# Performance work log

Hardware: AMD Instinct MI355X
Metric: run time of the kernel (lower is better)

## Reference

```python
import jax, jax.numpy as jnp
import numpy as np

E, N, D = 800000, 50000, 64

def setup_inputs() -> dict:
    key = jax.random.key(0)
    k0, k1, k2, k3 = jax.random.split(key, 4)
    return {
        "edge_attrs": jax.random.normal(k0, (E, D), dtype=jnp.float32),
        "proj_W": jax.random.normal(k1, (D, D), dtype=jnp.float32) / np.float32(np.sqrt(D)),
        "proj_b": jnp.zeros((D,), dtype=jnp.float32),
        "upd_W": jax.random.normal(k2, (D, D), dtype=jnp.float32) / np.float32(np.sqrt(D)),
        "upd_b": jnp.zeros((D,), dtype=jnp.float32),
        "dst": jax.random.randint(k3, (E,), 0, N, dtype=jnp.int32),
        "n_nodes": N,
    }

def reference(edge_attrs, proj_W, proj_b, upd_W, upd_b, dst, n_nodes):
    # Project each edge attribute: node_projectors[e.type](e.data)
    proj = edge_attrs @ proj_W + proj_b                      # [E, D]
    # Mean-aggregate incoming edges per destination node (MeanAggregator)
    summed = jax.ops.segment_sum(proj, dst, num_segments=n_nodes)          # [N, D]
    counts = jax.ops.segment_sum(jnp.ones((dst.shape[0], 1), proj.dtype),
                                 dst, num_segments=n_nodes)                # [N, 1]
    aggregated = summed / jnp.maximum(counts, 1.0)           # nodes w/o edges -> 0
    # Per-node update: updaters(aggregated)
    return aggregated @ upd_W + upd_b                        # [N, D]
```

## Files before the change

### kernel.cpp

```cpp
#include <hip/hip_runtime.h>
#include <hip/hip_bf16.h>

#define D 64

typedef float f32x4 __attribute__((ext_vector_type(4)));

__global__ void zero_kernel(int4* __restrict__ p, int n4) {
    int i = blockIdx.x * blockDim.x + threadIdx.x;
    if (i < n4) p[i] = make_int4(0, 0, 0, 0);
}

__global__ void count_kernel(const int4* __restrict__ dst4, int* __restrict__ counts, int E4) {
    int i = blockIdx.x * blockDim.x + threadIdx.x;
    if (i < E4) {
        int4 d = dst4[i];
        atomicAdd(&counts[d.x], 1);
        atomicAdd(&counts[d.y], 1);
        atomicAdd(&counts[d.z], 1);
        atomicAdd(&counts[d.w], 1);
    }
}

__global__ void blocksum_kernel(const int* __restrict__ counts, int* __restrict__ bsums, int N) {
    int t = threadIdx.x;
    int i = blockIdx.x * 256 + t;
    int v = (i < N) ? counts[i] : 0;
    int lane = t & 63, wave = t >> 6;
    #pragma unroll
    for (int o = 1; o < 64; o <<= 1) v += __shfl_xor(v, o);
    __shared__ int ws[4];
    if (lane == 0) ws[wave] = v;
    __syncthreads();
    if (t == 0) bsums[blockIdx.x] = ws[0] + ws[1] + ws[2] + ws[3];
}

__global__ void blockscan_kernel(const int* __restrict__ bsums, int* __restrict__ boffs,
                                 int* __restrict__ offsets, int N, int nb,
                                 const float* __restrict__ Wp, const float* __restrict__ Wu,
                                 const float* __restrict__ bp,
                                 float* __restrict__ Wc, float* __restrict__ bc) {
    __shared__ int wsum[16];
    __shared__ float wu[D * D];
    __shared__ float wp[D * D];
    int t = threadIdx.x;
    for (int i = t; i < D * D; i += 1024) { wu[i] = Wu[i]; wp[i] = Wp[i]; }

    int wave = t >> 6, lane = t & 63;
    int v = (t < nb) ? bsums[t] : 0;
    int s = v;
    #pragma unroll
    for (int off = 1; off < 64; off <<= 1) {
        int x = __shfl_up(s, off);
        if (lane >= off) s += x;
    }
    if (lane == 63) wsum[wave] = s;
    __syncthreads();
    int wbase = 0, total = 0;
    #pragma unroll
    for (int w = 0; w < 16; ++w) {
        int x = wsum[w];
        total += x;
        if (w < wave) wbase += x;
    }
    if (t < nb) boffs[t] = s - v + wbase;
    if (t == 0) offsets[N] = total;

    for (int idx = t; idx < D * D; idx += 1024) {
        int d = idx >> 6, j = idx & 63;
        float acc = 0.f;
        #pragma unroll
        for (int k = 0; k < D; ++k) acc = fmaf(wp[d * D + k], wu[k * D + j], acc);
        Wc[idx] = acc;
    }
    if (t < D) {
        float acc = 0.f;
        #pragma unroll
        for (int k = 0; k < D; ++k) acc = fmaf(bp[k], wu[k * D + t], acc);
        bc[t] = acc;
    }
}

__global__ void scatter_scan_kernel(const int* __restrict__ counts, const int* __restrict__ boffs,
                                    int* __restrict__ offsets, int* __restrict__ cursor, int N) {
    int t = threadIdx.x;
    int i = blockIdx.x * 256 + t;
    int v = (i < N) ? counts[i] : 0;
    int lane = t & 63, wave = t >> 6;
    int s = v;
    #pragma unroll
    for (int off = 1; off < 64; off <<= 1) {
        int x = __shfl_up(s, off);
        if (lane >= off) s += x;
    }
    __shared__ int ws[4];
    if (lane == 63) ws[wave] = s;
    __syncthreads();
    int wbase = 0;
    #pragma unroll
    for (int w = 0; w < 4; ++w) if (w < wave) wbase += ws[w];
    int excl = s - v + wbase + boffs[blockIdx.x];
    if (i < N) { offsets[i] = excl; cursor[i] = excl; }
}

__global__ void fill_kernel(const int4* __restrict__ dst4, int* __restrict__ cursor,
                            int* __restrict__ csr, int E4) {
    int i = blockIdx.x * blockDim.x + threadIdx.x;
    if (i < E4) {
        int4 d = dst4[i];
        int e = i * 4;
        csr[atomicAdd(&cursor[d.x], 1)] = e + 0;
        csr[atomicAdd(&cursor[d.y], 1)] = e + 1;
        csr[atomicAdd(&cursor[d.z], 1)] = e + 2;
        csr[atomicAdd(&cursor[d.w], 1)] = e + 3;
    }
}

__global__ __launch_bounds__(256) void node_kernel(
        const f32x4* __restrict__ attrs4, const int* __restrict__ csr,
        const int* __restrict__ offsets,
        const float* __restrict__ Wc, const float* __restrict__ bc,
        const float* __restrict__ ub, float* __restrict__ out, int N) {
    __shared__ float wlds[D * D];
    __shared__ float blds[D];
    __shared__ float ulds[D];
    __shared__ int soff[5];
    int t = threadIdx.x;
    int nbase = blockIdx.x * 4;
    if (t < 5) {
        int nn = nbase + t;
        soff[t] = offsets[(nn <= N) ? nn : N];
    }
    #pragma unroll
    for (int i = t; i < D * D; i += 256) wlds[i] = Wc[i];
    if (t < D) { blds[t] = bc[t]; ulds[t] = ub[t]; }
    __syncthreads();

    int wave = t >> 6, lane = t & 63;
    int n = nbase + wave;
    if (n >= N) return;

    int off = soff[wave];
    int cnt = soff[wave + 1] - off;

    int g = lane >> 4;
    int q = lane & 15;

    f32x4 acc0 = (f32x4)(0.f), acc1 = (f32x4)(0.f), acc2 = (f32x4)(0.f), acc3 = (f32x4)(0.f);
    for (int base = 0; base < cnt; base += 64) {
        int m = cnt - base; if (m > 64) m = 64;
        int idxv = (lane < m) ? __builtin_nontemporal_load(&csr[off + base + lane]) : 0;
        int jj = 0;
        for (; jj + 16 <= m; jj += 16) {
            int e0 = __shfl(idxv, jj + g);
            int e1 = __shfl(idxv, jj + 4 + g);
            int e2 = __shfl(idxv, jj + 8 + g);
            int e3 = __shfl(idxv, jj + 12 + g);
            f32x4 a0 = __builtin_nontemporal_load(&attrs4[(size_t)e0 * 16 + q]);
            f32x4 a1 = __builtin_nontemporal_load(&attrs4[(size_t)e1 * 16 + q]);
            f32x4 a2 = __builtin_nontemporal_load(&attrs4[(size_t)e2 * 16 + q]);
            f32x4 a3 = __builtin_nontemporal_load(&attrs4[(size_t)e3 * 16 + q]);
            acc0 += a0; acc1 += a1; acc2 += a2; acc3 += a3;
        }
        for (; jj + 8 <= m; jj += 8) {
            int e0 = __shfl(idxv, jj + g);
            int e1 = __shfl(idxv, jj + 4 + g);
            f32x4 a0 = __builtin_nontemporal_load(&attrs4[(size_t)e0 * 16 + q]);
            f32x4 a1 = __builtin_nontemporal_load(&attrs4[(size_t)e1 * 16 + q]);
            acc0 += a0; acc1 += a1;
        }
        for (; jj < m; jj += 4) {
            int sel = jj + g;
            int e = __shfl(idxv, sel);
            if (sel < m) {
                f32x4 a = __builtin_nontemporal_load(&attrs4[(size_t)e * 16 + q]);
                acc0 += a;
            }
        }
    }
    f32x4 acc = (acc0 + acc1) + (acc2 + acc3);
    acc.x += __shfl_xor(acc.x, 16); acc.y += __shfl_xor(acc.y, 16);
    acc.z += __shfl_xor(acc.z, 16); acc.w += __shfl_xor(acc.w, 16);
    acc.x += __shfl_xor(acc.x, 32); acc.y += __shfl_xor(acc.y, 32);
    acc.z += __shfl_xor(acc.z, 32); acc.w += __shfl_xor(acc.w, 32);

    float inv = (cnt > 0) ? 1.f / (float)cnt : 0.f;
    float marr[4] = { acc.x * inv, acc.y * inv, acc.z * inv, acc.w * inv };

    float accO = ulds[lane] + ((cnt > 0) ? blds[lane] : 0.f);
    #pragma unroll
    for (int d = 0; d < D; ++d) {
        float mv = __shfl(marr[d & 3], d >> 2);
        accO = fmaf(mv, wlds[d * D + lane], accO);
    }
    out[(size_t)n * D + lane] = accO;
}

extern "C" void kernel_launch(void* const* d_in, const int* in_sizes, int n_in,
                              void* d_out, int out_size, void* d_ws, size_t ws_size,
                              hipStream_t stream) {
    const float* edge_attrs = (const float*)d_in[0];
    const float* proj_W     = (const float*)d_in[1];
    const float* proj_b     = (const float*)d_in[2];
    const float* upd_W      = (const float*)d_in[3];
    const float* upd_b      = (const float*)d_in[4];
    const int*   dst        = (const int*)d_in[5];

    const int E = in_sizes[0] / D;
    const int N = out_size / D;
    const int nb = (N + 255) / 256;
    const int E4 = E / 4;
    const int N4 = N / 4;

    int*   counts  = (int*)d_ws;
    int*   offsets = counts + N;
    int*   cursor  = offsets + N + 1;
    int*   bsums   = cursor + N;
    int*   boffs   = bsums + nb;
    int*   csr     = boffs + nb;
    float* Wc      = (float*)(csr + E);
    float* bc      = Wc + D * D;

    zero_kernel<<<(N4 + 255) / 256, 256, 0, stream>>>((int4*)counts, N4);
    count_kernel<<<(E4 + 255) / 256, 256, 0, stream>>>((const int4*)dst, counts, E4);
    blocksum_kernel<<<nb, 256, 0, stream>>>(counts, bsums, N);
    blockscan_kernel<<<1, 1024, 0, stream>>>(bsums, boffs, offsets, N, nb,
                                             proj_W, upd_W, proj_b, Wc, bc);
    scatter_scan_kernel<<<nb, 256, 0, stream>>>(counts, boffs, offsets, cursor, N);
    fill_kernel<<<(E4 + 255) / 256, 256, 0, stream>>>((const int4*)dst, cursor, csr, E4);

    int blocks_n = (N + 3) / 4;
    node_kernel<<<blocks_n, 256, 0, stream>>>((const f32x4*)edge_attrs, csr, offsets,
                                              Wc, bc, upd_b, (float*)d_out, N);
}
```

Baseline: 173.9 us.

## Scatter edge attributes into destination-sorted bf16 buffer before node aggregation

```diff
diff --git a/kernel.cpp b/kernel.cpp
--- a/kernel.cpp
+++ b/kernel.cpp
@@ -4,6 +4,7 @@
 #define D 64
 
 typedef float f32x4 __attribute__((ext_vector_type(4)));
+typedef float f32x2 __attribute__((ext_vector_type(2)));
 
 __global__ void zero_kernel(int4* __restrict__ p, int n4) {
     int i = blockIdx.x * blockDim.x + threadIdx.x;
@@ -102,21 +103,28 @@
     if (i < N) { offsets[i] = excl; cursor[i] = excl; }
 }
 
-__global__ void fill_kernel(const int4* __restrict__ dst4, int* __restrict__ cursor,
-                            int* __restrict__ csr, int E4) {
-    int i = blockIdx.x * blockDim.x + threadIdx.x;
-    if (i < E4) {
-        int4 d = dst4[i];
-        int e = i * 4;
-        csr[atomicAdd(&cursor[d.x], 1)] = e + 0;
-        csr[atomicAdd(&cursor[d.y], 1)] = e + 1;
-        csr[atomicAdd(&cursor[d.z], 1)] = e + 2;
-        csr[atomicAdd(&cursor[d.w], 1)] = e + 3;
+__global__ __launch_bounds__(256) void scatter_bf16_kernel(
+        const f32x2* __restrict__ attrs2, const int* __restrict__ dst,
+        int* __restrict__ cursor, ushort2* __restrict__ ebuf, int E) {
+    int lane = threadIdx.x & 63;
+    int stride = gridDim.x * 256;
+    int E32 = E * 32;
+    for (int t = blockIdx.x * 256 + threadIdx.x; t < E32; t += stride) {
+        int e = t >> 5, j = t & 31;
+        f32x2 v = __builtin_nontemporal_load(&attrs2[t]);
+        int pos = 0;
+        if ((lane & 31) == 0) pos = atomicAdd(&cursor[dst[e]], 1);
+        pos = __shfl(pos, lane & 32);
+        unsigned ux = __float_as_uint(v.x);
+        unsigned uy = __float_as_uint(v.y);
+        ux = (ux + 0x7fffu + ((ux >> 16) & 1u)) >> 16;
+        uy = (uy + 0x7fffu + ((uy >> 16) & 1u)) >> 16;
+        ebuf[(size_t)pos * 32 + j] = make_ushort2((unsigned short)ux, (unsigned short)uy);
     }
 }
 
 __global__ __launch_bounds__(256) void node_kernel(
-        const f32x4* __restrict__ attrs4, const int* __restrict__ csr,
+        const f32x4* __restrict__ ebuf4,
         const int* __restrict__ offsets,
         const float* __restrict__ Wc, const float* __restrict__ bc,
         const float* __restrict__ ub, float* __restrict__ out, int N) {
@@ -140,56 +148,42 @@
     if (n >= N) return;
 
     int off = soff[wave];
-    int cnt = soff[wave + 1] - off;
-
-    int g = lane >> 4;
-    int q = lane & 15;
-
-    f32x4 acc0 = (f32x4)(0.f), acc1 = (f32x4)(0.f), acc2 = (f32x4)(0.f), acc3 = (f32x4)(0.f);
-    for (int base = 0; base < cnt; base += 64) {
-        int m = cnt - base; if (m > 64) m = 64;
-        int idxv = (lane < m) ? __builtin_nontemporal_load(&csr[off + base + lane]) : 0;
-        int jj = 0;
-        for (; jj + 16 <= m; jj += 16) {
-            int e0 = __shfl(idxv, jj + g);
-            int e1 = __shfl(idxv, jj + 4 + g);
-            int e2 = __shfl(idxv, jj + 8 + g);
-            int e3 = __shfl(idxv, jj + 12 + g);
-            f32x4 a0 = __builtin_nontemporal_load(&attrs4[(size_t)e0 * 16 + q]);
-            f32x4 a1 = __builtin_nontemporal_load(&attrs4[(size_t)e1 * 16 + q]);
-            f32x4 a2 = __builtin_nontemporal_load(&attrs4[(size_t)e2 * 16 + q]);
-            f32x4 a3 = __builtin_nontemporal_load(&attrs4[(size_t)e3 * 16 + q]);
-            acc0 += a0; acc1 += a1; acc2 += a2; acc3 += a3;
+    int off2 = soff[wave + 1];
+    int cnt = off2 - off;
+
+    int rsel = lane >> 3;
+    int csel = lane & 7;
+
+    float a0 = 0.f, a1 = 0.f, a2 = 0.f, a3 = 0.f, a4 = 0.f, a5 = 0.f, a6 = 0.f, a7 = 0.f;
+    for (int r0 = off; r0 < off2; r0 += 8) {
+        int row = r0 + rsel;
+        bool valid = row < off2;
+        int idx = (valid ? row : off) * 8 + csel;
+        f32x4 c = ebuf4[idx];
+        if (valid) {
+            unsigned u0 = __float_as_uint(c.x), u1 = __float_as_uint(c.y);
+            unsigned u2 = __float_as_uint(c.z), u3 = __float_as_uint(c.w);
+            a0 += __uint_as_float(u0 << 16); a1 += __uint_as_float(u0 & 0xffff0000u);
+            a2 += __uint_as_float(u1 << 16); a3 += __uint_as_float(u1 & 0xffff0000u);
+            a4 += __uint_as_float(u2 << 16); a5 += __uint_as_float(u2 & 0xffff0000u);
+            a6 += __uint_as_float(u3 << 16); a7 += __uint_as_float(u3 & 0xffff0000u);
         }
-        for (; jj + 8 <= m; jj += 8) {
-            int e0 = __shfl(idxv, jj + g);
-            int e1 = __shfl(idxv, jj + 4 + g);
-            f32x4 a0 = __builtin_nontemporal_load(&attrs4[(size_t)e0 * 16 + q]);
-            f32x4 a1 = __builtin_nontemporal_load(&attrs4[(size_t)e1 * 16 + q]);
-            acc0 += a0; acc1 += a1;
-        }
-        for (; jj < m; jj += 4) {
-            int sel = jj + g;
-            int e = __shfl(idxv, sel);
-            if (sel < m) {
-                f32x4 a = __builtin_nontemporal_load(&attrs4[(size_t)e * 16 + q]);
-                acc0 += a;
-            }
-        }
-    }
-    f32x4 acc = (acc0 + acc1) + (acc2 + acc3);
-    acc.x += __shfl_xor(acc.x, 16); acc.y += __shfl_xor(acc.y, 16);
-    acc.z += __shfl_xor(acc.z, 16); acc.w += __shfl_xor(acc.w, 16);
-    acc.x += __shfl_xor(acc.x, 32); acc.y += __shfl_xor(acc.y, 32);
-    acc.z += __shfl_xor(acc.z, 32); acc.w += __shfl_xor(acc.w, 32);
-
+    }
+    #pragma unroll
+    for (int mask = 8; mask < 64; mask <<= 1) {
+        a0 += __shfl_xor(a0, mask); a1 += __shfl_xor(a1, mask);
+        a2 += __shfl_xor(a2, mask); a3 += __shfl_xor(a3, mask);
+        a4 += __shfl_xor(a4, mask); a5 += __shfl_xor(a5, mask);
+        a6 += __shfl_xor(a6, mask); a7 += __shfl_xor(a7, mask);
+    }
     float inv = (cnt > 0) ? 1.f / (float)cnt : 0.f;
-    float marr[4] = { acc.x * inv, acc.y * inv, acc.z * inv, acc.w * inv };
+    float marr[8] = { a0 * inv, a1 * inv, a2 * inv, a3 * inv,
+                      a4 * inv, a5 * inv, a6 * inv, a7 * inv };
 
     float accO = ulds[lane] + ((cnt > 0) ? blds[lane] : 0.f);
     #pragma unroll
     for (int d = 0; d < D; ++d) {
-        float mv = __shfl(marr[d & 3], d >> 2);
+        float mv = __shfl(marr[d & 7], d >> 3);
         accO = fmaf(mv, wlds[d * D + lane], accO);
     }
     out[(size_t)n * D + lane] = accO;
@@ -216,9 +210,10 @@
     int*   cursor  = offsets + N + 1;
     int*   bsums   = cursor + N;
     int*   boffs   = bsums + nb;
-    int*   csr     = boffs + nb;
-    float* Wc      = (float*)(csr + E);
+    float* Wc      = (float*)(boffs + nb);
     float* bc      = Wc + D * D;
+    size_t ebuf_off = (((size_t)(bc + D) - (size_t)d_ws) + 255) & ~(size_t)255;
+    ushort2* ebuf   = (ushort2*)((char*)d_ws + ebuf_off);
 
     zero_kernel<<<(N4 + 255) / 256, 256, 0, stream>>>((int4*)counts, N4);
     count_kernel<<<(E4 + 255) / 256, 256, 0, stream>>>((const int4*)dst, counts, E4);
@@ -226,9 +221,10 @@
     blockscan_kernel<<<1, 1024, 0, stream>>>(bsums, boffs, offsets, N, nb,
                                              proj_W, upd_W, proj_b, Wc, bc);
     scatter_scan_kernel<<<nb, 256, 0, stream>>>(counts, boffs, offsets, cursor, N);
-    fill_kernel<<<(E4 + 255) / 256, 256, 0, stream>>>((const int4*)dst, cursor, csr, E4);
+    scatter_bf16_kernel<<<2048, 256, 0, stream>>>((const f32x2*)edge_attrs, dst,
+                                                  cursor, ebuf, E);
 
     int blocks_n = (N + 3) / 4;
-    node_kernel<<<blocks_n, 256, 0, stream>>>((const f32x4*)edge_attrs, csr, offsets,
+    node_kernel<<<blocks_n, 256, 0, stream>>>((const f32x4*)ebuf, offsets,
                                               Wc, bc, upd_b, (float*)d_out, N);
 }
```

Result: slower. 195.9 us (+12.6%).
